# Optimization experiments

Measured on AMD Instinct MI355X. Metric: run time of the kernel, lower is better.

The kernel has to match this reference:

```python
import jax, jax.numpy as jnp
import numpy as np

INPUT_DIM = 512
OUTPUT_DIM = 512
NUM_BASIS = 16
GRID_MIN, GRID_MAX = -2.0, 2.0
LN_EPS = 1e-5


def rbf_basis(x):
    # x: [batch, input_dim] -> [batch, input_dim, num_basis]
    centers = jnp.linspace(GRID_MIN, GRID_MAX, NUM_BASIS, dtype=x.dtype)  # [K]
    h = (GRID_MAX - GRID_MIN) / (NUM_BASIS - 1)
    z = (x[..., None] - centers) / h
    return jnp.exp(-(z * z))


def setup_inputs() -> dict:
    key = jax.random.key(0)
    k1, k2, k3 = jax.random.split(key, 3)
    x = jax.random.normal(k1, (4096, INPUT_DIM), dtype=jnp.float32)
    weights = jax.random.normal(k2, (OUTPUT_DIM, INPUT_DIM, NUM_BASIS), dtype=jnp.float32) * 0.1
    base_weights = jax.random.normal(k3, (OUTPUT_DIM, INPUT_DIM), dtype=jnp.float32) * 0.1
    ln_gamma = jnp.ones((OUTPUT_DIM,), dtype=jnp.float32)
    ln_beta = jnp.zeros((OUTPUT_DIM,), dtype=jnp.float32)
    return {"x": x, "weights": weights, "base_weights": base_weights,
            "ln_gamma": ln_gamma, "ln_beta": ln_beta}


def reference(x, weights, base_weights, ln_gamma, ln_beta):
    # per-edge basis expansion: [B, I, K]
    basis = rbf_basis(x)
    # fused contraction replacing the nested python loops:
    # out[b, j] = sum_{i,k} basis[b, i, k] * weights[j, i, k]
    out = jnp.einsum('bik,jik->bj', basis, weights)
    # residual base activation path
    out = out + jax.nn.silu(x) @ base_weights.T
    # layer norm over output_dim
    mean = jnp.mean(out, axis=-1, keepdims=True)
    var = jnp.var(out, axis=-1, keepdims=True)
    out = (out - mean) * jax.lax.rsqrt(var + LN_EPS) * ln_gamma + ln_beta
    return out
```

## Files before the change

### kernel.cpp

```cpp
#include <hip/hip_runtime.h>
#include <hip/hip_bf16.h>


typedef __bf16 bf16x8 __attribute__((ext_vector_type(8)));
typedef __bf16 bf16x4 __attribute__((ext_vector_type(4)));
typedef float  f32x4  __attribute__((ext_vector_type(4)));

#define KT 8704
#define SPLITS 8
#define KS (KT / SPLITS)
#define NIT (KS / 32)
#define CPE (4096 * 512)
#define LBUF (128 * 32)

__device__ __forceinline__ void gll16(const __bf16* g, __bf16* l) {
    __builtin_amdgcn_global_load_lds(
        (const __attribute__((address_space(1))) void*)g,
        (__attribute__((address_space(3))) void*)l, 16, 0, 0);
}

__global__ void prep_AB(const float* __restrict__ x, const float* __restrict__ W,
                        const float* __restrict__ Wb, __bf16* __restrict__ A,
                        __bf16* __restrict__ B) {
    if (blockIdx.x < 8192) {
        int t = blockIdx.x * 256 + threadIdx.x;
        int b = t >> 9;
        int i = t & 511;
        float xv = x[t];
        float zb = 3.75f * xv + 7.5f;
        bf16x8 lo, hi;
#pragma unroll
        for (int k = 0; k < 8; ++k) { float z = zb - (float)k; lo[k]   = (__bf16)__expf(-z * z); }
#pragma unroll
        for (int k = 8; k < 16; ++k){ float z = zb - (float)k; hi[k-8] = (__bf16)__expf(-z * z); }
        size_t base = (size_t)b * KT + (size_t)i * 16;
        *(bf16x8*)(A + base)     = lo;
        *(bf16x8*)(A + base + 8) = hi;
        float s = xv / (1.0f + __expf(-xv));
        A[(size_t)b * KT + 8192 + i] = (__bf16)s;
    } else {
        int t = (blockIdx.x - 8192) * 256 + threadIdx.x;
        int j = t / 2176;
        int c = (t - j * 2176) * 4;
        float4 v;
        if (c < 8192) v = *(const float4*)&W[(size_t)j * 8192 + c];
        else          v = *(const float4*)&Wb[(size_t)j * 512 + (c - 8192)];
        bf16x4 o;
        o[0] = (__bf16)v.x; o[1] = (__bf16)v.y; o[2] = (__bf16)v.z; o[3] = (__bf16)v.w;
        *(bf16x4*)&B[(size_t)j * KT + c] = o;
    }
}

__global__ __launch_bounds__(256, 4) void gemm_bt(const __bf16* __restrict__ A,
                                                  const __bf16* __restrict__ B,
                                                  __bf16* __restrict__ Cp) {
    __shared__ __attribute__((aligned(16))) __bf16 As[2 * LBUF];
    __shared__ __attribute__((aligned(16))) __bf16 Bs[2 * LBUF];

    const int tid  = threadIdx.x;
    const int wave = tid >> 6, lane = tid & 63;
    const int q    = lane >> 4, r16 = lane & 15;
    const int m0 = blockIdx.x * 128, n0 = blockIdx.y * 128, k0 = blockIdx.z * KS;
    const int wm = wave & 1, wn = wave >> 1;

    const int row0 = tid >> 2, qk0 = (tid & 3) ^ ((row0 >> 1) & 3);
    const int row1 = row0 + 64, qk1 = (tid & 3) ^ ((row1 >> 1) & 3);
    const __bf16* gA0 = A + (size_t)(m0 + row0) * KT + k0 + qk0 * 8;
    const __bf16* gA1 = A + (size_t)(m0 + row1) * KT + k0 + qk1 * 8;
    const __bf16* gB0 = B + (size_t)(n0 + row0) * KT + k0 + qk0 * 8;
    const __bf16* gB1 = B + (size_t)(n0 + row1) * KT + k0 + qk1 * 8;

    f32x4 acc[4][4] = {};

    const int qa = q ^ ((r16 >> 1) & 3);
    const int awOff = (wm * 64 + r16) * 32 + qa * 8;
    const int bwOff = (wn * 64 + r16) * 32 + qa * 8;

    gll16(gA0, &As[tid * 8]);
    gll16(gA1, &As[(tid + 256) * 8]);
    gll16(gB0, &Bs[tid * 8]);
    gll16(gB1, &Bs[(tid + 256) * 8]);
    __syncthreads();

    for (int it = 0; it < NIT; ++it) {
        const int ko = (it + 1) * 32;
        const int sb = ((it + 1) & 1) * LBUF;
        gll16(gA0 + ko, &As[sb + tid * 8]);
        gll16(gA1 + ko, &As[sb + (tid + 256) * 8]);
        gll16(gB0 + ko, &Bs[sb + tid * 8]);
        gll16(gB1 + ko, &Bs[sb + (tid + 256) * 8]);

        const int cb = (it & 1) * LBUF;
        const __bf16* Aw = &As[cb + awOff];
        const __bf16* Bw = &Bs[cb + bwOff];
        bf16x8 af[4], bg[4];
#pragma unroll
        for (int mi = 0; mi < 4; ++mi) af[mi] = *(const bf16x8*)(Aw + mi * 512);
#pragma unroll
        for (int ni = 0; ni < 4; ++ni) bg[ni] = *(const bf16x8*)(Bw + ni * 512);
#pragma unroll
        for (int mi = 0; mi < 4; ++mi)
#pragma unroll
            for (int ni = 0; ni < 4; ++ni)
                acc[mi][ni] = __builtin_amdgcn_mfma_f32_16x16x32_bf16(
                    af[mi], bg[ni], acc[mi][ni], 0, 0, 0);

        __syncthreads();
    }

    __bf16* Cb = Cp + (size_t)blockIdx.z * CPE;
#pragma unroll
    for (int mi = 0; mi < 4; ++mi) {
        const int row = m0 + wm * 64 + mi * 16 + q * 4;
#pragma unroll
        for (int ni = 0; ni < 4; ++ni) {
            const int col = n0 + wn * 64 + ni * 16 + r16;
#pragma unroll
            for (int r = 0; r < 4; ++r)
                Cb[(size_t)(row + r) * 512 + col] = (__bf16)acc[mi][ni][r];
        }
    }
}

__global__ void ln_kernel(const __bf16* __restrict__ Cp, const float* __restrict__ gamma,
                          const float* __restrict__ beta, float* __restrict__ out) {
    const int tid  = threadIdx.x;
    const int wave = tid >> 6, lane = tid & 63;
    const int row  = blockIdx.x * 4 + wave;
    const size_t base = (size_t)row * 512 + lane * 8;

    float v[8] = {};
    float s = 0.f, s2 = 0.f;
#pragma unroll
    for (int z = 0; z < SPLITS; ++z) {
        bf16x8 p = *(const bf16x8*)(Cp + (size_t)z * CPE + base);
#pragma unroll
        for (int j = 0; j < 8; ++j) v[j] += (float)p[j];
    }
#pragma unroll
    for (int j = 0; j < 8; ++j) { s += v[j]; s2 += v[j] * v[j]; }
#pragma unroll
    for (int m = 32; m >= 1; m >>= 1) {
        s  += __shfl_xor(s, m);
        s2 += __shfl_xor(s2, m);
    }
    const float mean = s * (1.0f / 512.0f);
    const float var  = s2 * (1.0f / 512.0f) - mean * mean;
    const float rs   = rsqrtf(var + 1e-5f);
    float4 o0, o1;
    const float4 g0 = *(const float4*)&gamma[lane * 8];
    const float4 g1 = *(const float4*)&gamma[lane * 8 + 4];
    const float4 b0 = *(const float4*)&beta[lane * 8];
    const float4 b1 = *(const float4*)&beta[lane * 8 + 4];
    o0.x = (v[0] - mean) * rs * g0.x + b0.x;
    o0.y = (v[1] - mean) * rs * g0.y + b0.y;
    o0.z = (v[2] - mean) * rs * g0.z + b0.z;
    o0.w = (v[3] - mean) * rs * g0.w + b0.w;
    o1.x = (v[4] - mean) * rs * g1.x + b1.x;
    o1.y = (v[5] - mean) * rs * g1.y + b1.y;
    o1.z = (v[6] - mean) * rs * g1.z + b1.z;
    o1.w = (v[7] - mean) * rs * g1.w + b1.w;
    *(float4*)&out[base]     = o0;
    *(float4*)&out[base + 4] = o1;
}

extern "C" void kernel_launch(void* const* d_in, const int* in_sizes, int n_in,
                              void* d_out, int out_size, void* d_ws, size_t ws_size,
                              hipStream_t stream) {
    const float* x     = (const float*)d_in[0];
    const float* W     = (const float*)d_in[1];
    const float* Wb    = (const float*)d_in[2];
    const float* gamma = (const float*)d_in[3];
    const float* beta  = (const float*)d_in[4];
    float* out = (float*)d_out;

    char* ws = (char*)d_ws;
    __bf16* A  = (__bf16*)ws;
    __bf16* Bm = (__bf16*)(ws + 71303168);
    __bf16* Cp = (__bf16*)(ws + 80216064);

    prep_AB<<<8192 + 4352, 256, 0, stream>>>(x, W, Wb, A, Bm);
    dim3 g(32, 4, SPLITS);
    gemm_bt<<<g, 256, 0, stream>>>(A, Bm, Cp);
    ln_kernel<<<1024, 256, 0, stream>>>(Cp, gamma, beta, out);
}
```

Before: 143.5 us.

## Fuse RBF and SiLU basis generation into GEMM A-tile loading

Measured after the change: 144.1 us. No clear change (+0.4%).

```diff
diff --git a/kernel.cpp b/kernel.cpp
--- a/kernel.cpp
+++ b/kernel.cpp
@@ -8,8 +8,7 @@
 
 #define KT 8704
 #define SPLITS 8
-#define KS (KT / SPLITS)
-#define NIT (KS / 32)
+#define NIT 34
 #define CPE (4096 * 512)
 #define LBUF (128 * 32)
 
@@ -19,77 +18,106 @@
         (__attribute__((address_space(3))) void*)l, 16, 0, 0);
 }
 
-__global__ void prep_AB(const float* __restrict__ x, const float* __restrict__ W,
-                        const float* __restrict__ Wb, __bf16* __restrict__ A,
-                        __bf16* __restrict__ B) {
-    if (blockIdx.x < 8192) {
-        int t = blockIdx.x * 256 + threadIdx.x;
-        int b = t >> 9;
-        int i = t & 511;
-        float xv = x[t];
-        float zb = 3.75f * xv + 7.5f;
-        bf16x8 lo, hi;
-#pragma unroll
-        for (int k = 0; k < 8; ++k) { float z = zb - (float)k; lo[k]   = (__bf16)__expf(-z * z); }
-#pragma unroll
-        for (int k = 8; k < 16; ++k){ float z = zb - (float)k; hi[k-8] = (__bf16)__expf(-z * z); }
-        size_t base = (size_t)b * KT + (size_t)i * 16;
-        *(bf16x8*)(A + base)     = lo;
-        *(bf16x8*)(A + base + 8) = hi;
-        float s = xv / (1.0f + __expf(-xv));
-        A[(size_t)b * KT + 8192 + i] = (__bf16)s;
-    } else {
-        int t = (blockIdx.x - 8192) * 256 + threadIdx.x;
-        int j = t / 2176;
-        int c = (t - j * 2176) * 4;
-        float4 v;
-        if (c < 8192) v = *(const float4*)&W[(size_t)j * 8192 + c];
-        else          v = *(const float4*)&Wb[(size_t)j * 512 + (c - 8192)];
-        bf16x4 o;
-        o[0] = (__bf16)v.x; o[1] = (__bf16)v.y; o[2] = (__bf16)v.z; o[3] = (__bf16)v.w;
-        *(bf16x4*)&B[(size_t)j * KT + c] = o;
-    }
-}
-
-__global__ __launch_bounds__(256, 4) void gemm_bt(const __bf16* __restrict__ A,
-                                                  const __bf16* __restrict__ B,
-                                                  __bf16* __restrict__ Cp) {
+__device__ __forceinline__ float fsilu(float t) {
+    return t * __builtin_amdgcn_rcpf(1.0f + __expf(-t));
+}
+
+__global__ void prep_B(const float* __restrict__ W, const float* __restrict__ Wb,
+                       __bf16* __restrict__ B) {
+    int t = blockIdx.x * 256 + threadIdx.x;
+    int j = t / 2176;
+    int c = (t - j * 2176) * 4;
+    float4 v;
+    if (c < 8192) v = *(const float4*)&W[(size_t)j * 8192 + c];
+    else          v = *(const float4*)&Wb[(size_t)j * 512 + (c - 8192)];
+    bf16x4 o;
+    o[0] = (__bf16)v.x; o[1] = (__bf16)v.y; o[2] = (__bf16)v.z; o[3] = (__bf16)v.w;
+    *(bf16x4*)&B[(size_t)j * KT + c] = o;
+}
+
+__global__ __launch_bounds__(256, 4) void gemm_fused(const float* __restrict__ x,
+                                                     const __bf16* __restrict__ B,
+                                                     __bf16* __restrict__ Cp) {
     __shared__ __attribute__((aligned(16))) __bf16 As[2 * LBUF];
     __shared__ __attribute__((aligned(16))) __bf16 Bs[2 * LBUF];
 
     const int tid  = threadIdx.x;
     const int wave = tid >> 6, lane = tid & 63;
     const int q    = lane >> 4, r16 = lane & 15;
-    const int m0 = blockIdx.x * 128, n0 = blockIdx.y * 128, k0 = blockIdx.z * KS;
+    const int m0 = blockIdx.x * 128, n0 = blockIdx.y * 128;
+    const int bz = blockIdx.z, k0 = bz * 1088;
     const int wm = wave & 1, wn = wave >> 1;
+    const bool zlast = (bz == SPLITS - 1);
 
     const int row0 = tid >> 2, qk0 = (tid & 3) ^ ((row0 >> 1) & 3);
     const int row1 = row0 + 64, qk1 = (tid & 3) ^ ((row1 >> 1) & 3);
-    const __bf16* gA0 = A + (size_t)(m0 + row0) * KT + k0 + qk0 * 8;
-    const __bf16* gA1 = A + (size_t)(m0 + row1) * KT + k0 + qk1 * 8;
     const __bf16* gB0 = B + (size_t)(n0 + row0) * KT + k0 + qk0 * 8;
     const __bf16* gB1 = B + (size_t)(n0 + row1) * KT + k0 + qk1 * 8;
 
+    const int arow = tid >> 1, p = tid & 1;
+    const int sw = (arow >> 1) & 3;
+    const int c0 = arow * 4 + ((2 * p)     ^ sw);
+    const int c1 = arow * 4 + ((2 * p + 1) ^ sw);
+    const float* xr = x + (size_t)(m0 + arow) * 512;
+    const int i0 = bz * 68;
+
     f32x4 acc[4][4] = {};
-
     const int qa = q ^ ((r16 >> 1) & 3);
     const int awOff = (wm * 64 + r16) * 32 + qa * 8;
     const int bwOff = (wn * 64 + r16) * 32 + qa * 8;
 
-    gll16(gA0, &As[tid * 8]);
-    gll16(gA1, &As[(tid + 256) * 8]);
-    gll16(gB0, &Bs[tid * 8]);
-    gll16(gB1, &Bs[(tid + 256) * 8]);
+    {
+        float xv = xr[i0 + p];
+        float zb = 3.75f * xv + 7.5f;
+        bf16x8 v;
+#pragma unroll
+        for (int j = 0; j < 8; ++j) { float d = zb - (float)j; v[j] = (__bf16)__expf(-d * d); }
+        *(bf16x8*)&As[c0 * 8] = v;
+#pragma unroll
+        for (int j = 8; j < 16; ++j) { float d = zb - (float)j; v[j - 8] = (__bf16)__expf(-d * d); }
+        *(bf16x8*)&As[c1 * 8] = v;
+        gll16(gB0, &Bs[tid * 8]);
+        gll16(gB1, &Bs[(tid + 256) * 8]);
+    }
+    float xv_pipe = xr[i0 + 2 + p];
     __syncthreads();
 
     for (int it = 0; it < NIT; ++it) {
-        const int ko = (it + 1) * 32;
-        const int sb = ((it + 1) & 1) * LBUF;
-        gll16(gA0 + ko, &As[sb + tid * 8]);
-        gll16(gA1 + ko, &As[sb + (tid + 256) * 8]);
-        gll16(gB0 + ko, &Bs[sb + tid * 8]);
-        gll16(gB1 + ko, &Bs[sb + (tid + 256) * 8]);
-
+        const int itn = it + 1;
+        if (itn < NIT) {
+            const int sb = (itn & 1) * LBUF;
+            gll16(gB0 + itn * 32, &Bs[sb + tid * 8]);
+            gll16(gB1 + itn * 32, &Bs[sb + (tid + 256) * 8]);
+            if (zlast && itn >= 18) {
+                const int c = (itn - 18) * 32 + p * 16;
+                float4 a0 = *(const float4*)&xr[c];
+                float4 a1 = *(const float4*)&xr[c + 4];
+                bf16x8 v;
+                v[0] = (__bf16)fsilu(a0.x); v[1] = (__bf16)fsilu(a0.y);
+                v[2] = (__bf16)fsilu(a0.z); v[3] = (__bf16)fsilu(a0.w);
+                v[4] = (__bf16)fsilu(a1.x); v[5] = (__bf16)fsilu(a1.y);
+                v[6] = (__bf16)fsilu(a1.z); v[7] = (__bf16)fsilu(a1.w);
+                *(bf16x8*)&As[sb + c0 * 8] = v;
+                float4 a2 = *(const float4*)&xr[c + 8];
+                float4 a3 = *(const float4*)&xr[c + 12];
+                v[0] = (__bf16)fsilu(a2.x); v[1] = (__bf16)fsilu(a2.y);
+                v[2] = (__bf16)fsilu(a2.z); v[3] = (__bf16)fsilu(a2.w);
+                v[4] = (__bf16)fsilu(a3.x); v[5] = (__bf16)fsilu(a3.y);
+                v[6] = (__bf16)fsilu(a3.z); v[7] = (__bf16)fsilu(a3.w);
+                *(bf16x8*)&As[sb + c1 * 8] = v;
+            } else {
+                float zb = 3.75f * xv_pipe + 7.5f;
+                bf16x8 v;
+#pragma unroll
+                for (int j = 0; j < 8; ++j) { float d = zb - (float)j; v[j] = (__bf16)__expf(-d * d); }
+                *(bf16x8*)&As[sb + c0 * 8] = v;
+#pragma unroll
+                for (int j = 8; j < 16; ++j) { float d = zb - (float)j; v[j - 8] = (__bf16)__expf(-d * d); }
+                *(bf16x8*)&As[sb + c1 * 8] = v;
+                if (itn + 1 < NIT && !(zlast && itn + 1 >= 18))
+                    xv_pipe = xr[i0 + (itn + 1) * 2 + p];
+            }
+        }
         const int cb = (it & 1) * LBUF;
         const __bf16* Aw = &As[cb + awOff];
         const __bf16* Bw = &Bs[cb + bwOff];
@@ -104,11 +132,10 @@
             for (int ni = 0; ni < 4; ++ni)
                 acc[mi][ni] = __builtin_amdgcn_mfma_f32_16x16x32_bf16(
                     af[mi], bg[ni], acc[mi][ni], 0, 0, 0);
-
         __syncthreads();
     }
 
-    __bf16* Cb = Cp + (size_t)blockIdx.z * CPE;
+    __bf16* Cb = Cp + (size_t)bz * CPE;
 #pragma unroll
     for (int mi = 0; mi < 4; ++mi) {
         const int row = m0 + wm * 64 + mi * 16 + q * 4;
@@ -133,9 +160,9 @@
     float s = 0.f, s2 = 0.f;
 #pragma unroll
     for (int z = 0; z < SPLITS; ++z) {
-        bf16x8 p = *(const bf16x8*)(Cp + (size_t)z * CPE + base);
-#pragma unroll
-        for (int j = 0; j < 8; ++j) v[j] += (float)p[j];
+        bf16x8 pv = *(const bf16x8*)(Cp + (size_t)z * CPE + base);
+#pragma unroll
+        for (int j = 0; j < 8; ++j) v[j] += (float)pv[j];
     }
 #pragma unroll
     for (int j = 0; j < 8; ++j) { s += v[j]; s2 += v[j] * v[j]; }
@@ -175,12 +202,11 @@
     float* out = (float*)d_out;
 
     char* ws = (char*)d_ws;
-    __bf16* A  = (__bf16*)ws;
-    __bf16* Bm = (__bf16*)(ws + 71303168);
-    __bf16* Cp = (__bf16*)(ws + 80216064);
-
-    prep_AB<<<8192 + 4352, 256, 0, stream>>>(x, W, Wb, A, Bm);
+    __bf16* Bm = (__bf16*)ws;
+    __bf16* Cp = (__bf16*)(ws + 8912896);
+
+    prep_B<<<4352, 256, 0, stream>>>(W, Wb, Bm);
     dim3 g(32, 4, SPLITS);
-    gemm_bt<<<g, 256, 0, stream>>>(A, Bm, Cp);
+    gemm_fused<<<g, 256, 0, stream>>>(x, Bm, Cp);
     ln_kernel<<<1024, 256, 0, stream>>>(Cp, gamma, beta, out);
 }
```

## Load B fragments directly from global in pre-swizzled slab layout, drop B LDS staging

Applied to the files above, without the earlier changes.

Measured after the change: 148.4 us. +3.4%, slower.

```diff
diff --git a/kernel.cpp b/kernel.cpp
--- a/kernel.cpp
+++ b/kernel.cpp
@@ -8,10 +8,10 @@
 
 #define KT 8704
 #define SPLITS 8
-#define KS (KT / SPLITS)
-#define NIT (KS / 32)
+#define NIT 34
 #define CPE (4096 * 512)
 #define LBUF (128 * 32)
+#define BSLAB 16384
 
 __device__ __forceinline__ void gll16(const __bf16* g, __bf16* l) {
     __builtin_amdgcn_global_load_lds(
@@ -19,11 +19,16 @@
         (__attribute__((address_space(3))) void*)l, 16, 0, 0);
 }
 
-__global__ void prep_AB(const float* __restrict__ x, const float* __restrict__ W,
-                        const float* __restrict__ Wb, __bf16* __restrict__ A,
-                        __bf16* __restrict__ B) {
-    if (blockIdx.x < 8192) {
-        int t = blockIdx.x * 256 + threadIdx.x;
+__device__ __forceinline__ float fsilu(float t) {
+    return t * __builtin_amdgcn_rcpf(1.0f + __expf(-t));
+}
+
+__global__ void prep_all(const float* __restrict__ x, const float* __restrict__ W,
+                         const float* __restrict__ Wb, __bf16* __restrict__ A,
+                         __bf16* __restrict__ B2) {
+    const int blk = blockIdx.x, tid = threadIdx.x;
+    if (blk < 8192) {
+        int t = blk * 256 + tid;
         int b = t >> 9;
         int i = t & 511;
         float xv = x[t];
@@ -36,10 +41,9 @@
         size_t base = (size_t)b * KT + (size_t)i * 16;
         *(bf16x8*)(A + base)     = lo;
         *(bf16x8*)(A + base + 8) = hi;
-        float s = xv / (1.0f + __expf(-xv));
-        A[(size_t)b * KT + 8192 + i] = (__bf16)s;
+        A[(size_t)b * KT + 8192 + i] = (__bf16)fsilu(xv);
     } else {
-        int t = (blockIdx.x - 8192) * 256 + threadIdx.x;
+        int t = (blk - 8192) * 256 + tid;
         int j = t / 2176;
         int c = (t - j * 2176) * 4;
         float4 v;
@@ -47,57 +51,56 @@
         else          v = *(const float4*)&Wb[(size_t)j * 512 + (c - 8192)];
         bf16x4 o;
         o[0] = (__bf16)v.x; o[1] = (__bf16)v.y; o[2] = (__bf16)v.z; o[3] = (__bf16)v.w;
-        *(bf16x4*)&B[(size_t)j * KT + c] = o;
+        *(bf16x4*)(B2 + ((size_t)(c >> 5) * 512 + j) * 32 + (c & 31)) = o;
     }
 }
 
-__global__ __launch_bounds__(256, 4) void gemm_bt(const __bf16* __restrict__ A,
-                                                  const __bf16* __restrict__ B,
-                                                  __bf16* __restrict__ Cp) {
+__global__ __launch_bounds__(256, 4) void gemm_hyb(const __bf16* __restrict__ A,
+                                                   const __bf16* __restrict__ B2,
+                                                   __bf16* __restrict__ Cp) {
     __shared__ __attribute__((aligned(16))) __bf16 As[2 * LBUF];
-    __shared__ __attribute__((aligned(16))) __bf16 Bs[2 * LBUF];
 
     const int tid  = threadIdx.x;
     const int wave = tid >> 6, lane = tid & 63;
     const int q    = lane >> 4, r16 = lane & 15;
-    const int m0 = blockIdx.x * 128, n0 = blockIdx.y * 128, k0 = blockIdx.z * KS;
+    const int m0 = blockIdx.x * 128, n0 = blockIdx.y * 128;
+    const int bz = blockIdx.z, k0 = bz * 1088, slab0 = bz * NIT;
     const int wm = wave & 1, wn = wave >> 1;
 
     const int row0 = tid >> 2, qk0 = (tid & 3) ^ ((row0 >> 1) & 3);
     const int row1 = row0 + 64, qk1 = (tid & 3) ^ ((row1 >> 1) & 3);
     const __bf16* gA0 = A + (size_t)(m0 + row0) * KT + k0 + qk0 * 8;
     const __bf16* gA1 = A + (size_t)(m0 + row1) * KT + k0 + qk1 * 8;
-    const __bf16* gB0 = B + (size_t)(n0 + row0) * KT + k0 + qk0 * 8;
-    const __bf16* gB1 = B + (size_t)(n0 + row1) * KT + k0 + qk1 * 8;
+
+    const __bf16* bBase = B2 + (size_t)slab0 * BSLAB
+                        + (size_t)(n0 + wn * 64 + r16) * 32 + q * 8;
 
     f32x4 acc[4][4] = {};
-
     const int qa = q ^ ((r16 >> 1) & 3);
     const int awOff = (wm * 64 + r16) * 32 + qa * 8;
-    const int bwOff = (wn * 64 + r16) * 32 + qa * 8;
 
     gll16(gA0, &As[tid * 8]);
     gll16(gA1, &As[(tid + 256) * 8]);
-    gll16(gB0, &Bs[tid * 8]);
-    gll16(gB1, &Bs[(tid + 256) * 8]);
     __syncthreads();
 
     for (int it = 0; it < NIT; ++it) {
-        const int ko = (it + 1) * 32;
-        const int sb = ((it + 1) & 1) * LBUF;
-        gll16(gA0 + ko, &As[sb + tid * 8]);
-        gll16(gA1 + ko, &As[sb + (tid + 256) * 8]);
-        gll16(gB0 + ko, &Bs[sb + tid * 8]);
-        gll16(gB1 + ko, &Bs[sb + (tid + 256) * 8]);
+        bf16x8 bg[4];
+        const __bf16* bp = bBase + (size_t)it * BSLAB;
+#pragma unroll
+        for (int ni = 0; ni < 4; ++ni) bg[ni] = *(const bf16x8*)(bp + ni * 512);
 
-        const int cb = (it & 1) * LBUF;
-        const __bf16* Aw = &As[cb + awOff];
-        const __bf16* Bw = &Bs[cb + bwOff];
-        bf16x8 af[4], bg[4];
+        if (it + 1 < NIT) {
+            const int go = (it + 1) * 32;
+            const int sb = ((it + 1) & 1) * LBUF;
+            gll16(gA0 + go, &As[sb + tid * 8]);
+            gll16(gA1 + go, &As[sb + (tid + 256) * 8]);
+        }
+
+        const __bf16* Aw = &As[(it & 1) * LBUF + awOff];
+        bf16x8 af[4];
 #pragma unroll
         for (int mi = 0; mi < 4; ++mi) af[mi] = *(const bf16x8*)(Aw + mi * 512);
-#pragma unroll
-        for (int ni = 0; ni < 4; ++ni) bg[ni] = *(const bf16x8*)(Bw + ni * 512);
+
 #pragma unroll
         for (int mi = 0; mi < 4; ++mi)
 #pragma unroll
@@ -108,7 +111,7 @@
         __syncthreads();
     }
 
-    __bf16* Cb = Cp + (size_t)blockIdx.z * CPE;
+    __bf16* Cb = Cp + (size_t)bz * CPE;
 #pragma unroll
     for (int mi = 0; mi < 4; ++mi) {
         const int row = m0 + wm * 64 + mi * 16 + q * 4;
@@ -133,9 +136,9 @@
     float s = 0.f, s2 = 0.f;
 #pragma unroll
     for (int z = 0; z < SPLITS; ++z) {
-        bf16x8 p = *(const bf16x8*)(Cp + (size_t)z * CPE + base);
+        bf16x8 pv = *(const bf16x8*)(Cp + (size_t)z * CPE + base);
 #pragma unroll
-        for (int j = 0; j < 8; ++j) v[j] += (float)p[j];
+        for (int j = 0; j < 8; ++j) v[j] += (float)pv[j];
     }
 #pragma unroll
     for (int j = 0; j < 8; ++j) { s += v[j]; s2 += v[j] * v[j]; }
@@ -176,11 +179,11 @@
 
     char* ws = (char*)d_ws;
     __bf16* A  = (__bf16*)ws;
-    __bf16* Bm = (__bf16*)(ws + 71303168);
+    __bf16* B2 = (__bf16*)(ws + 71303168);
     __bf16* Cp = (__bf16*)(ws + 80216064);
 
-    prep_AB<<<8192 + 4352, 256, 0, stream>>>(x, W, Wb, A, Bm);
+    prep_all<<<8192 + 4352, 256, 0, stream>>>(x, W, Wb, A, B2);
     dim3 g(32, 4, SPLITS);
-    gemm_bt<<<g, 256, 0, stream>>>(A, Bm, Cp);
+    gemm_hyb<<<g, 256, 0, stream>>>(A, B2, Cp);
     ln_kernel<<<1024, 256, 0, stream>>>(Cp, gamma, beta, out);
 }
```
